# Performance work log

Hardware: AMD Instinct MI355X
Metric: run time of the kernel (lower is better)

Reference implementation:

```python
import jax, jax.numpy as jnp
import numpy as np

EPS = 1e-8  # F.cosine_similarity default eps


def setup_inputs() -> dict:
    key = jax.random.key(0)
    k1, k2, k3, k4 = jax.random.split(key, 4)
    Q, P, E, V = 4096, 16384, 128, 30000
    query = jax.random.randint(k1, (Q,), 0, V, dtype=jnp.int64)
    para = jax.random.randint(k2, (P,), 0, V, dtype=jnp.int64)
    que_embed = jax.random.normal(k3, (Q, E), dtype=jnp.float32)
    para_embed = jax.random.normal(k4, (P, E), dtype=jnp.float32)
    return {"query": query, "para": para, "que_embed": que_embed, "para_embed": para_embed}


def reference(query, para, que_embed, para_embed):
    # xor_matrix[i, j] = 1 if query[i] == para[j] else 0  -> [Q, P] int64
    xor_matrix = (query[:, None] == para[None, :]).astype(jnp.int64)
    # cos_matrix[i, j] = cosine_similarity(que_embed[i], para_embed[j])
    # torch semantics: dot / (max(||q||, eps) * max(||p||, eps))
    q_norm = jnp.maximum(jnp.linalg.norm(que_embed, axis=-1), EPS)   # [Q]
    p_norm = jnp.maximum(jnp.linalg.norm(para_embed, axis=-1), EPS)  # [P]
    dots = jnp.einsum('qe,pe->qp', que_embed, para_embed)            # [Q, P]
    cos_matrix = dots / (q_norm[:, None] * p_norm[None, :])
    return xor_matrix, cos_matrix
```

## Files before the change

### kernel.cpp

```cpp
#include <hip/hip_runtime.h>
#include <stdint.h>

typedef __attribute__((ext_vector_type(8))) short bf16x8;
typedef __attribute__((ext_vector_type(4))) float f32x4;

__device__ __forceinline__ uint32_t f2bf(float f) {
    uint32_t u = __builtin_bit_cast(uint32_t, f);
    u += 0x7fffu + ((u >> 16) & 1u);
    return u >> 16;
}
__device__ __forceinline__ uint32_t pack2(float a, float b) {
    return f2bf(a) | (f2bf(b) << 16);
}

__global__ __launch_bounds__(256) void prep_all(const float* __restrict__ qe,
                                                const float* __restrict__ pe,
                                                unsigned short* __restrict__ Qf,
                                                unsigned short* __restrict__ Pf,
                                                float* __restrict__ rq,
                                                float* __restrict__ rp,
                                                int qgroups) {
    __shared__ float part[16][17];
    const int gi = blockIdx.x;
    const int rem = threadIdx.x;
    const bool isQ = gi < qgroups;
    const int g = isQ ? gi : gi - qgroups;
    const float* src = isQ ? qe : pe;
    unsigned short* dst = isQ ? Qf : Pf;

    const int c = rem >> 6, lane = rem & 63;
    const int rowl = lane & 15;
    const int hi = lane >> 4;
    const int row = g * 16 + rowl;
    const int col = c * 32 + hi * 8;
    const float* s = src + (size_t)row * 128 + col;
    float4 a0 = *(const float4*)s;
    float4 a1 = *(const float4*)(s + 4);
    uint4 pk = { pack2(a0.x, a0.y), pack2(a0.z, a0.w),
                 pack2(a1.x, a1.y), pack2(a1.z, a1.w) };
    *(uint4*)(dst + ((size_t)g * 256 + rem) * 8) = pk;

    float ssq = a0.x*a0.x + a0.y*a0.y + a0.z*a0.z + a0.w*a0.w
              + a1.x*a1.x + a1.y*a1.y + a1.z*a1.z + a1.w*a1.w;
    part[rowl][c * 4 + hi] = ssq;
    __syncthreads();
    if (rem < 16) {
        float s16 = 0.f;
#pragma unroll
        for (int j = 0; j < 16; ++j) s16 += part[rem][j];
        float r = 1.0f / fmaxf(sqrtf(s16), 1e-8f);
        (isQ ? rq : rp)[g * 16 + rem] = r;
    }
}

__global__ __launch_bounds__(256) void xor_stream(const int* __restrict__ qid,
                                                  const int* __restrict__ pid,
                                                  float* __restrict__ oxor,
                                                  int total4, int pmask_log2) {
    const int stride = gridDim.x * 256;
    int idx = blockIdx.x * 256 + threadIdx.x;
    const int pmask = (1 << pmask_log2) - 1;
    for (; idx < total4; idx += stride) {
        const int q = idx >> pmask_log2;
        const int pi = (idx & pmask) << 2;
        const int qv = qid[q];
        const int4 pv = *(const int4*)(pid + pi);
        f32x4 x = { pv.x == qv ? 1.f : 0.f, pv.y == qv ? 1.f : 0.f,
                    pv.z == qv ? 1.f : 0.f, pv.w == qv ? 1.f : 0.f };
        __builtin_nontemporal_store(x, (f32x4*)(oxor + ((size_t)idx << 2)));
    }
}

#define PBLK 2048

__global__ __launch_bounds__(256, 4) void cos_gemm(
        const unsigned short* __restrict__ Qf, const unsigned short* __restrict__ Pf,
        const float* __restrict__ rq, const float* __restrict__ rp,
        float* __restrict__ ocos, int Pn) {
    __shared__ __align__(16) float scos[4][16][68];

    const int nwg = gridDim.x;
    const int chunk = nwg >> 3;
    const int bid = blockIdx.x;
    const int wg = (bid & 7) * chunk + (bid >> 3);
    const int nPc = Pn / PBLK;
    const int qg = wg / nPc;
    const int pc = wg % nPc;
    const int pblock = pc * PBLK;

    const int t = threadIdx.x;
    const int lane = t & 63;
    const int w = t >> 6;
    const int lq = lane & 15;
    const int g4 = (lane >> 4) << 2;

    bf16x8 af[4];
    const unsigned short* abase = Qf + (size_t)qg * 2048 + lane * 8;
#pragma unroll
    for (int kk = 0; kk < 4; ++kk)
        af[kk] = *(const bf16x8*)(abase + kk * 512);

    const int qrow_base = qg * 16;
    const float rqv = rq[qrow_base + lq];

    for (int fl = 0; fl < PBLK / 256; ++fl) {
        const int pw = pblock + fl * 256 + w * 64;
#pragma unroll
        for (int f = 0; f < 4; ++f) {
            const int p0 = pw + f * 16;
            const unsigned short* bbase = Pf + (size_t)(p0 >> 4) * 2048 + (size_t)lane * 8;
            bf16x8 bfr[4];
#pragma unroll
            for (int kk = 0; kk < 4; ++kk)
                bfr[kk] = *(const bf16x8*)(bbase + kk * 512);
            f32x4 acc = {0.f, 0.f, 0.f, 0.f};
#pragma unroll
            for (int kk = 0; kk < 4; ++kk)
                acc = __builtin_amdgcn_mfma_f32_16x16x32_bf16(bfr[kk], af[kk], acc, 0, 0, 0);
            const float4 rpv = *(const float4*)(rp + p0 + g4);
            f32x4 c4 = { acc[0]*rqv*rpv.x, acc[1]*rqv*rpv.y,
                         acc[2]*rqv*rpv.z, acc[3]*rqv*rpv.w };
            *(f32x4*)&scos[w][lq][f * 16 + g4] = c4;
        }
#pragma unroll
        for (int r = 0; r < 16; ++r) {
            float vc = scos[w][r][lane];
            __builtin_nontemporal_store(vc,
                ocos + (size_t)(qrow_base + r) * Pn + pw + lane);
        }
    }
}

extern "C" void kernel_launch(void* const* d_in, const int* in_sizes, int n_in,
                              void* d_out, int out_size, void* d_ws, size_t ws_size,
                              hipStream_t stream) {
    const int*   qid = (const int*)d_in[0];
    const int*   pid = (const int*)d_in[1];
    const float* qe  = (const float*)d_in[2];
    const float* pe  = (const float*)d_in[3];
    const int Q  = in_sizes[0];
    const int Pn = in_sizes[1];

    unsigned short* Qf = (unsigned short*)d_ws;
    unsigned short* Pf = Qf + (size_t)Q * 128;
    float* rq = (float*)(Pf + (size_t)Pn * 128);
    float* rp = rq + Q;

    float* oxor = (float*)d_out;
    float* ocos = oxor + (size_t)Q * (size_t)Pn;

    const int qgroups = Q / 16, pgroups = Pn / 16;
    prep_all<<<qgroups + pgroups, 256, 0, stream>>>(qe, pe, Qf, Pf, rq, rp, qgroups);

    int lg = 0; while ((1 << lg) != Pn / 4) ++lg;
    const int total4 = (int)((size_t)Q * Pn / 4);
    xor_stream<<<2048, 256, 0, stream>>>(qid, pid, oxor, total4, lg);

    const int nblocks = (Q / 16) * (Pn / PBLK);
    cos_gemm<<<nblocks, 256, 0, stream>>>(Qf, Pf, rq, rp, ocos, Pn);
}
```

Before: 127.5 us.

## Fuse xor stream into cosine GEMM kernel with interleaved block roles

Merges the separate xor-matrix streaming kernel into the cosine GEMM launch: odd blocks write xor tiles while even blocks compute cosine tiles. The xor work is restructured so each block loads a pid vector once and reuses it across 32 query rows. This removes a kernel launch and lets memory-bound xor writes overlap with GEMM work on the same CUs. The cost is that heterogeneous blocks share launch bounds and occupancy.

```diff
diff --git a/kernel.cpp b/kernel.cpp
--- a/kernel.cpp
+++ b/kernel.cpp
@@ -53,44 +53,47 @@
     }
 }
 
-__global__ __launch_bounds__(256) void xor_stream(const int* __restrict__ qid,
-                                                  const int* __restrict__ pid,
-                                                  float* __restrict__ oxor,
-                                                  int total4, int pmask_log2) {
-    const int stride = gridDim.x * 256;
-    int idx = blockIdx.x * 256 + threadIdx.x;
-    const int pmask = (1 << pmask_log2) - 1;
-    for (; idx < total4; idx += stride) {
-        const int q = idx >> pmask_log2;
-        const int pi = (idx & pmask) << 2;
-        const int qv = qid[q];
-        const int4 pv = *(const int4*)(pid + pi);
-        f32x4 x = { pv.x == qv ? 1.f : 0.f, pv.y == qv ? 1.f : 0.f,
-                    pv.z == qv ? 1.f : 0.f, pv.w == qv ? 1.f : 0.f };
-        __builtin_nontemporal_store(x, (f32x4*)(oxor + ((size_t)idx << 2)));
-    }
-}
-
 #define PBLK 2048
 
-__global__ __launch_bounds__(256, 4) void cos_gemm(
+__global__ __launch_bounds__(256, 4) void fused_out(
         const unsigned short* __restrict__ Qf, const unsigned short* __restrict__ Pf,
+        const int* __restrict__ qid, const int* __restrict__ pid,
         const float* __restrict__ rq, const float* __restrict__ rp,
-        float* __restrict__ ocos, int Pn) {
+        float* __restrict__ oxor, float* __restrict__ ocos, int Pn) {
     __shared__ __align__(16) float scos[4][16][68];
 
-    const int nwg = gridDim.x;
+    const int bid = blockIdx.x;
+    const int t = threadIdx.x;
+    const int lane = t & 63;
+    const int w = t >> 6;
+
+    if (bid & 1) {
+        const int xb = bid >> 1;
+        const int nPw = Pn >> 10;
+        const int pw = (xb % nPw) * 1024 + w * 256 + lane * 4;
+        const int qb = (xb / nPw) * 32;
+        const int4 pv = *(const int4*)(pid + pw);
+        size_t obase = (size_t)qb * Pn + pw;
+#pragma unroll 8
+        for (int i = 0; i < 32; ++i) {
+            const int qv = qid[qb + i];
+            f32x4 x = { pv.x == qv ? 1.f : 0.f, pv.y == qv ? 1.f : 0.f,
+                        pv.z == qv ? 1.f : 0.f, pv.w == qv ? 1.f : 0.f };
+            __builtin_nontemporal_store(x, (f32x4*)(oxor + obase));
+            obase += (size_t)Pn;
+        }
+        return;
+    }
+
+    const int nwg = gridDim.x >> 1;
     const int chunk = nwg >> 3;
-    const int bid = blockIdx.x;
-    const int wg = (bid & 7) * chunk + (bid >> 3);
+    const int cb = bid >> 1;
+    const int wg = (cb & 7) * chunk + (cb >> 3);
     const int nPc = Pn / PBLK;
     const int qg = wg / nPc;
     const int pc = wg % nPc;
     const int pblock = pc * PBLK;
 
-    const int t = threadIdx.x;
-    const int lane = t & 63;
-    const int w = t >> 6;
     const int lq = lane & 15;
     const int g4 = (lane >> 4) << 2;
 
@@ -152,10 +155,6 @@
     const int qgroups = Q / 16, pgroups = Pn / 16;
     prep_all<<<qgroups + pgroups, 256, 0, stream>>>(qe, pe, Qf, Pf, rq, rp, qgroups);
 
-    int lg = 0; while ((1 << lg) != Pn / 4) ++lg;
-    const int total4 = (int)((size_t)Q * Pn / 4);
-    xor_stream<<<2048, 256, 0, stream>>>(qid, pid, oxor, total4, lg);
-
-    const int nblocks = (Q / 16) * (Pn / PBLK);
-    cos_gemm<<<nblocks, 256, 0, stream>>>(Qf, Pf, rq, rp, ocos, Pn);
+    const int nblocks = (Q / 16) * (Pn / PBLK) * 2;
+    fused_out<<<nblocks, 256, 0, stream>>>(Qf, Pf, qid, pid, rq, rp, oxor, ocos, Pn);
 }
```

After: 134.0 us. 1.05x slower.
